# Optimization experiments

Measured on AMD Instinct MI355X. Metric: run time of the kernel, lower is better.

## Reference

```python
import jax, jax.numpy as jnp
import numpy as np


def _phi(z, conv_w, conv_b):
    # z: (H, W, S, 1) -> 3x3 SAME conv over state channels -> softmax over states
    x = jnp.transpose(z[..., 0], (2, 0, 1))[None]  # (1, S, H, W)
    y = jax.lax.conv_general_dilated(
        x, conv_w, window_strides=(1, 1), padding='SAME',
        dimension_numbers=('NCHW', 'OIHW', 'NCHW')) + conv_b[None, :, None, None]
    return jax.nn.softmax(jnp.transpose(y[0], (1, 2, 0)), axis=2)[..., None]  # (H, W, S, 1)


def _update(obs, P, u_k, w_k_O, conv_w, conv_b):
    H, W, O = obs.shape
    S = P.shape[0]
    # b = P^T @ obs per cell: b[h,w,s] = sum_o P[o,s] * obs[h,w,o]
    b = jnp.einsum('os,hwo->hws', P, obs)[..., None]  # (H, W, S, 1)
    # Analytic Jacobian db/dP: deriv_b[h,w,s,0,i,j] = obs[h,w,i] * delta(s==j)
    eye = jnp.eye(S, O, dtype=obs.dtype)
    deriv_b = (obs[:, :, None, :, None] * eye[None, None, :, None, :])[:, :, :, None, :, :]  # (H,W,S,1,S,O)

    Bu = b * u_k                                  # (H, W, S, 1)
    bu = jnp.sum(Bu, axis=2, keepdims=True)       # (H, W, 1, 1)
    Z = Bu / bu                                   # Bu / bu

    u_kp1 = _phi(Z, conv_w, conv_b)               # (H, W, S, 1)

    # Sensitivity recursion for obs params (quotient rule on Bu/bu)
    du = deriv_b * u_k[..., None, None] + b[..., None, None] * w_k_O  # (H,W,S,1,S,O)
    term1 = du * bu[..., None, None]
    term2 = jnp.expand_dims(jnp.sum(du, axis=2), 3) * Bu[..., None, None]
    w_pre = (term1 - term2) / bu[..., None, None] ** 2                # (H,W,S,1,S,O)

    # J @ w  ==  9 JVPs of Phi at Z with tangent columns of w (exact, avoids dense (HWS)^2 Jacobian)
    tangents = jnp.moveaxis(w_pre.reshape(H, W, S, 1, S * O), -1, 0)  # (S*O, H, W, S, 1)
    jvp1 = lambda t: jax.jvp(lambda z: _phi(z, conv_w, conv_b), (Z,), (t,))[1]
    w_kp1_O = jnp.moveaxis(jax.vmap(jvp1)(tangents), 0, -1).reshape(H, W, S, 1, S, O)
    return u_kp1, w_kp1_O


def setup_inputs() -> dict:
    key = jax.random.key(0)
    k1, k2, k3 = jax.random.split(key, 3)
    H = W = 512
    S = O = 3
    obs = jax.random.uniform(k1, (H, W, O), dtype=jnp.float32)
    obs_param_matrix = jnp.ones((S, O), jnp.float32) / O          # row-stochastic init
    u_k = jnp.ones((H, W, S, 1), jnp.float32) / S                 # uniform belief
    w_k_O = jnp.zeros((H, W, S, 1, S, O), jnp.float32)
    conv_w = jax.random.normal(k2, (S, S, 3, 3), jnp.float32) * 0.1
    conv_b = jax.random.normal(k3, (S,), jnp.float32) * 0.1
    return {'obs': obs, 'obs_param_matrix': obs_param_matrix, 'u_k': u_k,
            'w_k_O': w_k_O, 'conv_w': conv_w, 'conv_b': conv_b}


def reference(obs, obs_param_matrix, u_k, w_k_O, conv_w, conv_b):
    return _update(obs, obs_param_matrix, u_k, w_k_O, conv_w, conv_b)
```

## Files before the change

### kernel.cpp

```cpp
#include <hip/hip_runtime.h>

#define IMH 512
#define IMW 512
#define TW 32
#define TH 8
#define HW_ (TW + 2)
#define HH_ (TH + 2)
#define NHALO (HW_ * HH_)
#define ROW 31

__global__ __launch_bounds__(256, 2)
void hmm_fused(const float* __restrict__ obs,
               const float* __restrict__ P,
               const float* __restrict__ u_k,
               const float* __restrict__ w_k,
               const float* __restrict__ conv_w,
               const float* __restrict__ conv_b,
               float* __restrict__ out) {
    __shared__ float lds[NHALO * ROW];

    const int tid = threadIdx.x;
    const int w0 = blockIdx.x * TW;
    const int h0 = blockIdx.y * TH;

    float Pm[9];
#pragma unroll
    for (int i = 0; i < 9; ++i) Pm[i] = P[i];

    for (int p = tid; p < NHALO; p += 256) {
        const int hh = h0 + p / HW_ - 1;
        const int ww = w0 + p % HW_ - 1;
        float* row = &lds[p * ROW];
        if (hh < 0 || hh >= IMH || ww < 0 || ww >= IMW) {
#pragma unroll
            for (int c = 0; c < 30; ++c) row[c] = 0.0f;
            continue;
        }
        const int pix = hh * IMW + ww;
        const float ov[3] = {obs[pix * 3 + 0], obs[pix * 3 + 1], obs[pix * 3 + 2]};
        const float us[3] = {u_k[pix * 3 + 0], u_k[pix * 3 + 1], u_k[pix * 3 + 2]};

        float b[3], Bu[3], bu = 0.0f;
#pragma unroll
        for (int s = 0; s < 3; ++s) {
            b[s] = Pm[0 * 3 + s] * ov[0] + Pm[1 * 3 + s] * ov[1] + Pm[2 * 3 + s] * ov[2];
            Bu[s] = b[s] * us[s];
            bu += Bu[s];
        }
        const float inv_bu = 1.0f / bu;
        float Z[3];
#pragma unroll
        for (int s = 0; s < 3; ++s) { Z[s] = Bu[s] * inv_bu; row[s] = Z[s]; }

        const float* wkp = &w_k[(size_t)pix * 27];
#pragma unroll
        for (int i = 0; i < 3; ++i) {
#pragma unroll
            for (int j = 0; j < 3; ++j) {
                const int ij = i * 3 + j;
                float du[3], sdu = 0.0f;
#pragma unroll
                for (int s = 0; s < 3; ++s) {
                    float d = b[s] * wkp[s * 9 + ij];
                    if (s == j) d += ov[i] * us[s];
                    du[s] = d;
                    sdu += d;
                }
#pragma unroll
                for (int s = 0; s < 3; ++s)
                    row[(1 + ij) * 3 + s] = (du[s] - sdu * Z[s]) * inv_bu;
            }
        }
    }

    float cw[81];
#pragma unroll
    for (int i = 0; i < 81; ++i) cw[i] = conv_w[i];
    const float cb[3] = {conv_b[0], conv_b[1], conv_b[2]};

    __syncthreads();

    const int tx = tid % TW, ty = tid / TW;
    const int hp = (ty + 1) * HW_ + (tx + 1);
    const int pix = (h0 + ty) * IMW + (w0 + tx);

    float p0, p1, p2;
    {
        float y[3] = {cb[0], cb[1], cb[2]};
#pragma unroll
        for (int ky = 0; ky < 3; ++ky) {
#pragma unroll
            for (int kx = 0; kx < 3; ++kx) {
                const float* nb = &lds[(hp + (ky - 1) * HW_ + (kx - 1)) * ROW];
                const float v0 = nb[0], v1 = nb[1], v2 = nb[2];
#pragma unroll
                for (int s = 0; s < 3; ++s)
                    y[s] += cw[s * 27 + 0 * 9 + ky * 3 + kx] * v0 +
                            cw[s * 27 + 1 * 9 + ky * 3 + kx] * v1 +
                            cw[s * 27 + 2 * 9 + ky * 3 + kx] * v2;
            }
        }
        const float m = fmaxf(y[0], fmaxf(y[1], y[2]));
        const float e0 = __expf(y[0] - m), e1 = __expf(y[1] - m), e2 = __expf(y[2] - m);
        const float inv = 1.0f / (e0 + e1 + e2);
        p0 = e0 * inv; p1 = e1 * inv; p2 = e2 * inv;
        out[pix * 3 + 0] = p0; out[pix * 3 + 1] = p1; out[pix * 3 + 2] = p2;
    }

    float wout[27];
#pragma unroll
    for (int g = 1; g < 10; ++g) {
        float a[3] = {0.0f, 0.0f, 0.0f};
#pragma unroll
        for (int ky = 0; ky < 3; ++ky) {
#pragma unroll
            for (int kx = 0; kx < 3; ++kx) {
                const float* nb = &lds[(hp + (ky - 1) * HW_ + (kx - 1)) * ROW];
                const float v0 = nb[g * 3 + 0], v1 = nb[g * 3 + 1], v2 = nb[g * 3 + 2];
#pragma unroll
                for (int s = 0; s < 3; ++s)
                    a[s] += cw[s * 27 + 0 * 9 + ky * 3 + kx] * v0 +
                            cw[s * 27 + 1 * 9 + ky * 3 + kx] * v1 +
                            cw[s * 27 + 2 * 9 + ky * 3 + kx] * v2;
            }
        }
        const float dot = p0 * a[0] + p1 * a[1] + p2 * a[2];
        const int ij = g - 1;
        wout[0 * 9 + ij] = p0 * (a[0] - dot);
        wout[1 * 9 + ij] = p1 * (a[1] - dot);
        wout[2 * 9 + ij] = p2 * (a[2] - dot);
    }

    __syncthreads();

#pragma unroll
    for (int c = 0; c < 27; ++c) lds[tid * 27 + c] = wout[c];
    __syncthreads();

    float* outw = out + IMH * IMW * 3;
    for (int idx = tid; idx < TW * TH * 27; idx += 256) {
        const int r = idx / (TW * 27);
        const int rem = idx - r * (TW * 27);
        outw[(h0 + r) * (IMW * 27) + w0 * 27 + rem] = lds[idx];
    }
}

extern "C" void kernel_launch(void* const* d_in, const int* in_sizes, int n_in,
                              void* d_out, int out_size, void* d_ws, size_t ws_size,
                              hipStream_t stream) {
    const float* obs    = (const float*)d_in[0];
    const float* P      = (const float*)d_in[1];
    const float* u_k    = (const float*)d_in[2];
    const float* w_k    = (const float*)d_in[3];
    const float* conv_w = (const float*)d_in[4];
    const float* conv_b = (const float*)d_in[5];
    float* out = (float*)d_out;

    dim3 grid(IMW / TW, IMH / TH);
    hmm_fused<<<grid, 256, 0, stream>>>(obs, P, u_k, w_k, conv_w, conv_b, out);
}
```

Measured before the change: 109.5 us.

## Coalesce w_k staging via LDS, swizzle float4 layout, single-pass conv accumulation

```diff
diff --git a/kernel.cpp b/kernel.cpp
--- a/kernel.cpp
+++ b/kernel.cpp
@@ -3,13 +3,13 @@
 #define IMH 512
 #define IMW 512
 #define TW 32
-#define TH 8
+#define TH 16
 #define HW_ (TW + 2)
 #define HH_ (TH + 2)
 #define NHALO (HW_ * HH_)
-#define ROW 31
+#define NTHR 512
 
-__global__ __launch_bounds__(256, 2)
+__global__ __launch_bounds__(NTHR, 4)
 void hmm_fused(const float* __restrict__ obs,
                const float* __restrict__ P,
                const float* __restrict__ u_k,
@@ -17,7 +17,8 @@
                const float* __restrict__ conv_w,
                const float* __restrict__ conv_b,
                float* __restrict__ out) {
-    __shared__ float lds[NHALO * ROW];
+    __shared__ float4 lds4[NHALO * 8];
+    float* lds = (float*)lds4;
 
     const int tid = threadIdx.x;
     const int w0 = blockIdx.x * TW;
@@ -27,108 +28,141 @@
 #pragma unroll
     for (int i = 0; i < 9; ++i) Pm[i] = P[i];
 
-    for (int p = tid; p < NHALO; p += 256) {
-        const int hh = h0 + p / HW_ - 1;
-        const int ww = w0 + p % HW_ - 1;
-        float* row = &lds[p * ROW];
-        if (hh < 0 || hh >= IMH || ww < 0 || ww >= IMW) {
-#pragma unroll
-            for (int c = 0; c < 30; ++c) row[c] = 0.0f;
-            continue;
-        }
-        const int pix = hh * IMW + ww;
-        const float ov[3] = {obs[pix * 3 + 0], obs[pix * 3 + 1], obs[pix * 3 + 2]};
-        const float us[3] = {u_k[pix * 3 + 0], u_k[pix * 3 + 1], u_k[pix * 3 + 2]};
-
-        float b[3], Bu[3], bu = 0.0f;
-#pragma unroll
-        for (int s = 0; s < 3; ++s) {
-            b[s] = Pm[0 * 3 + s] * ov[0] + Pm[1 * 3 + s] * ov[1] + Pm[2 * 3 + s] * ov[2];
-            Bu[s] = b[s] * us[s];
-            bu += Bu[s];
-        }
-        const float inv_bu = 1.0f / bu;
-        float Z[3];
-#pragma unroll
-        for (int s = 0; s < 3; ++s) { Z[s] = Bu[s] * inv_bu; row[s] = Z[s]; }
-
-        const float* wkp = &w_k[(size_t)pix * 27];
-#pragma unroll
-        for (int i = 0; i < 3; ++i) {
-#pragma unroll
-            for (int j = 0; j < 3; ++j) {
-                const int ij = i * 3 + j;
-                float du[3], sdu = 0.0f;
-#pragma unroll
-                for (int s = 0; s < 3; ++s) {
-                    float d = b[s] * wkp[s * 9 + ij];
-                    if (s == j) d += ov[i] * us[s];
-                    du[s] = d;
-                    sdu += d;
-                }
-#pragma unroll
-                for (int s = 0; s < 3; ++s)
-                    row[(1 + ij) * 3 + s] = (du[s] - sdu * Z[s]) * inv_bu;
-            }
+    for (int r = 0; r < HH_; ++r) {
+        const int hh = h0 + r - 1;
+        if (hh < 0 || hh >= IMH) continue;
+        const long long gbase = ((long long)hh * IMW + (w0 - 1)) * 27;
+        for (int f = tid; f < HW_ * 27; f += NTHR) {
+            const int p = f / 27;
+            const int c = f - p * 27;
+            const int ww = w0 - 1 + p;
+            float v = 0.0f;
+            if (ww >= 0 && ww < IMW) v = w_k[gbase + f];
+            const int pr = r * HW_ + p;
+            lds[pr * 32 + (((c >> 2) + pr) & 7) * 4 + (c & 3)] = v;
         }
     }
 
     float cw[81];
 #pragma unroll
     for (int i = 0; i < 81; ++i) cw[i] = conv_w[i];
-    const float cb[3] = {conv_b[0], conv_b[1], conv_b[2]};
+    const float cb0 = conv_b[0], cb1 = conv_b[1], cb2 = conv_b[2];
 
     __syncthreads();
 
-    const int tx = tid % TW, ty = tid / TW;
-    const int hp = (ty + 1) * HW_ + (tx + 1);
-    const int pix = (h0 + ty) * IMW + (w0 + tx);
+    for (int p = tid; p < NHALO; p += NTHR) {
+        const int rr = p / HW_;
+        const int cc = p - rr * HW_;
+        const int hh = h0 + rr - 1;
+        const int ww = w0 + cc - 1;
+        float4 o[8];
+        if ((unsigned)hh < IMH && (unsigned)ww < IMW) {
+            float wv[28];
+#pragma unroll
+            for (int k = 0; k < 7; ++k) {
+                const float4 v = lds4[p * 8 + ((k + p) & 7)];
+                wv[4 * k + 0] = v.x; wv[4 * k + 1] = v.y;
+                wv[4 * k + 2] = v.z; wv[4 * k + 3] = v.w;
+            }
+            const int pix = hh * IMW + ww;
+            const float ov0 = obs[pix * 3 + 0], ov1 = obs[pix * 3 + 1], ov2 = obs[pix * 3 + 2];
+            const float us[3] = {u_k[pix * 3 + 0], u_k[pix * 3 + 1], u_k[pix * 3 + 2]};
 
-    float p0, p1, p2;
-    {
-        float y[3] = {cb[0], cb[1], cb[2]};
+            float b[3], Bu[3], bu = 0.0f;
 #pragma unroll
-        for (int ky = 0; ky < 3; ++ky) {
+            for (int s = 0; s < 3; ++s) {
+                b[s] = Pm[0 * 3 + s] * ov0 + Pm[1 * 3 + s] * ov1 + Pm[2 * 3 + s] * ov2;
+                Bu[s] = b[s] * us[s];
+                bu += Bu[s];
+            }
+            const float inv_bu = 1.0f / bu;
+            float Z[3], oc[32];
 #pragma unroll
-            for (int kx = 0; kx < 3; ++kx) {
-                const float* nb = &lds[(hp + (ky - 1) * HW_ + (kx - 1)) * ROW];
-                const float v0 = nb[0], v1 = nb[1], v2 = nb[2];
+            for (int s = 0; s < 3; ++s) { Z[s] = Bu[s] * inv_bu; oc[s] = Z[s]; }
+
+            const float ovv[3] = {ov0, ov1, ov2};
 #pragma unroll
-                for (int s = 0; s < 3; ++s)
-                    y[s] += cw[s * 27 + 0 * 9 + ky * 3 + kx] * v0 +
-                            cw[s * 27 + 1 * 9 + ky * 3 + kx] * v1 +
-                            cw[s * 27 + 2 * 9 + ky * 3 + kx] * v2;
+            for (int i = 0; i < 3; ++i) {
+#pragma unroll
+                for (int j = 0; j < 3; ++j) {
+                    const int ij = i * 3 + j;
+                    float du[3], sdu = 0.0f;
+#pragma unroll
+                    for (int s = 0; s < 3; ++s) {
+                        float d = b[s] * wv[s * 9 + ij];
+                        if (s == j) d += ovv[i] * us[s];
+                        du[s] = d;
+                        sdu += d;
+                    }
+#pragma unroll
+                    for (int s = 0; s < 3; ++s)
+                        oc[3 + ij * 3 + s] = (du[s] - sdu * Z[s]) * inv_bu;
+                }
+            }
+            oc[30] = 0.0f; oc[31] = 0.0f;
+#pragma unroll
+            for (int k = 0; k < 8; ++k)
+                o[k] = make_float4(oc[4 * k + 0], oc[4 * k + 1], oc[4 * k + 2], oc[4 * k + 3]);
+        } else {
+#pragma unroll
+            for (int k = 0; k < 8; ++k) o[k] = make_float4(0.f, 0.f, 0.f, 0.f);
+        }
+#pragma unroll
+        for (int k = 0; k < 8; ++k) lds4[p * 8 + ((k + p) & 7)] = o[k];
+    }
+
+    __syncthreads();
+
+    const int tx = tid & (TW - 1);
+    const int ty = tid >> 5;
+    const int hp = (ty + 1) * HW_ + tx + 1;
+
+    float acc[30];
+#pragma unroll
+    for (int i = 0; i < 30; ++i) acc[i] = 0.0f;
+
+#pragma unroll
+    for (int ky = 0; ky < 3; ++ky) {
+#pragma unroll
+        for (int kx = 0; kx < 3; ++kx) {
+            const int tap = ky * 3 + kx;
+            const int pn = hp + (ky - 1) * HW_ + (kx - 1);
+#pragma unroll
+            for (int k = 0; k < 8; ++k) {
+                const float4 v4 = lds4[pn * 8 + ((k + pn) & 7)];
+                const float cv[4] = {v4.x, v4.y, v4.z, v4.w};
+#pragma unroll
+                for (int j = 0; j < 4; ++j) {
+                    const int c = 4 * k + j;
+                    if (c < 30) {
+                        const int g = c / 3, si = c - (c / 3) * 3;
+                        acc[g * 3 + 0] += cw[0 * 27 + si * 9 + tap] * cv[j];
+                        acc[g * 3 + 1] += cw[1 * 27 + si * 9 + tap] * cv[j];
+                        acc[g * 3 + 2] += cw[2 * 27 + si * 9 + tap] * cv[j];
+                    }
+                }
             }
         }
-        const float m = fmaxf(y[0], fmaxf(y[1], y[2]));
-        const float e0 = __expf(y[0] - m), e1 = __expf(y[1] - m), e2 = __expf(y[2] - m);
-        const float inv = 1.0f / (e0 + e1 + e2);
-        p0 = e0 * inv; p1 = e1 * inv; p2 = e2 * inv;
-        out[pix * 3 + 0] = p0; out[pix * 3 + 1] = p1; out[pix * 3 + 2] = p2;
     }
+
+    const float y0 = acc[0] + cb0, y1 = acc[1] + cb1, y2 = acc[2] + cb2;
+    const float m = fmaxf(y0, fmaxf(y1, y2));
+    const float e0 = __expf(y0 - m), e1 = __expf(y1 - m), e2 = __expf(y2 - m);
+    const float inv = 1.0f / (e0 + e1 + e2);
+    const float p0 = e0 * inv, p1 = e1 * inv, p2 = e2 * inv;
+
+    const int pix = (h0 + ty) * IMW + (w0 + tx);
+    out[pix * 3 + 0] = p0; out[pix * 3 + 1] = p1; out[pix * 3 + 2] = p2;
 
     float wout[27];
 #pragma unroll
     for (int g = 1; g < 10; ++g) {
-        float a[3] = {0.0f, 0.0f, 0.0f};
-#pragma unroll
-        for (int ky = 0; ky < 3; ++ky) {
-#pragma unroll
-            for (int kx = 0; kx < 3; ++kx) {
-                const float* nb = &lds[(hp + (ky - 1) * HW_ + (kx - 1)) * ROW];
-                const float v0 = nb[g * 3 + 0], v1 = nb[g * 3 + 1], v2 = nb[g * 3 + 2];
-#pragma unroll
-                for (int s = 0; s < 3; ++s)
-                    a[s] += cw[s * 27 + 0 * 9 + ky * 3 + kx] * v0 +
-                            cw[s * 27 + 1 * 9 + ky * 3 + kx] * v1 +
-                            cw[s * 27 + 2 * 9 + ky * 3 + kx] * v2;
-            }
-        }
-        const float dot = p0 * a[0] + p1 * a[1] + p2 * a[2];
+        const float a0 = acc[g * 3 + 0], a1 = acc[g * 3 + 1], a2 = acc[g * 3 + 2];
+        const float dot = p0 * a0 + p1 * a1 + p2 * a2;
         const int ij = g - 1;
-        wout[0 * 9 + ij] = p0 * (a[0] - dot);
-        wout[1 * 9 + ij] = p1 * (a[1] - dot);
-        wout[2 * 9 + ij] = p2 * (a[2] - dot);
+        wout[0 * 9 + ij] = p0 * (a0 - dot);
+        wout[1 * 9 + ij] = p1 * (a1 - dot);
+        wout[2 * 9 + ij] = p2 * (a2 - dot);
     }
 
     __syncthreads();
@@ -138,10 +172,12 @@
     __syncthreads();
 
     float* outw = out + IMH * IMW * 3;
-    for (int idx = tid; idx < TW * TH * 27; idx += 256) {
-        const int r = idx / (TW * 27);
-        const int rem = idx - r * (TW * 27);
-        outw[(h0 + r) * (IMW * 27) + w0 * 27 + rem] = lds[idx];
+    for (int idx = tid; idx < TW * TH * 27 / 4; idx += NTHR) {
+        const int r = idx / 216;
+        const int q = idx - r * 216;
+        const float4 v = lds4[r * 216 + q];
+        float4* dst = (float4*)(outw + ((size_t)(h0 + r) * IMW + w0) * 27);
+        dst[q] = v;
     }
 }
 
@@ -157,5 +193,5 @@
     float* out = (float*)d_out;
 
     dim3 grid(IMW / TW, IMH / TH);
-    hmm_fused<<<grid, 256, 0, stream>>>(obs, P, u_k, w_k, conv_w, conv_b, out);
+    hmm_fused<<<grid, NTHR, 0, stream>>>(obs, P, u_k, w_k, conv_w, conv_b, out);
 }
```

After: 125.6 us. +14.7%, slower.

## Split fused kernel into pointwise pass and planar-workspace conv pass

Applied to the files above, without the earlier changes.

```diff
diff --git a/kernel.cpp b/kernel.cpp
--- a/kernel.cpp
+++ b/kernel.cpp
@@ -2,146 +2,126 @@
 
 #define IMH 512
 #define IMW 512
-#define TW 32
-#define TH 8
-#define HW_ (TW + 2)
-#define HH_ (TH + 2)
-#define NHALO (HW_ * HH_)
-#define ROW 31
+#define NPIX (IMH * IMW)
+#define RS 516
+#define PR 514
+#define PLANE (PR * RS)
+#define NCH 30
+#define NBORD 2052
 
-__global__ __launch_bounds__(256, 2)
-void hmm_fused(const float* __restrict__ obs,
-               const float* __restrict__ P,
-               const float* __restrict__ u_k,
-               const float* __restrict__ w_k,
-               const float* __restrict__ conv_w,
-               const float* __restrict__ conv_b,
-               float* __restrict__ out) {
-    __shared__ float lds[NHALO * ROW];
+__global__ __launch_bounds__(256)
+void k1_pointwise(const float* __restrict__ obs,
+                  const float* __restrict__ P,
+                  const float* __restrict__ u_k,
+                  const float* __restrict__ w_k,
+                  float* __restrict__ ws) {
+    const int gtid = blockIdx.x * 256 + threadIdx.x;
 
-    const int tid = threadIdx.x;
-    const int w0 = blockIdx.x * TW;
-    const int h0 = blockIdx.y * TH;
+    for (int i = gtid; i < NCH * NBORD; i += NPIX) {
+        const int pl = i / NBORD, r = i - pl * NBORD;
+        int rr, cc;
+        if (r < 514)       { rr = 0;            cc = r; }
+        else if (r < 1028) { rr = 513;          cc = r - 514; }
+        else if (r < 1540) { rr = r - 1028 + 1; cc = 0; }
+        else               { rr = r - 1540 + 1; cc = 513; }
+        ws[(size_t)pl * PLANE + rr * RS + cc] = 0.0f;
+    }
 
-    float Pm[9];
+    const int h = gtid >> 9, w = gtid & 511;
+    const float ov[3] = {obs[gtid*3+0], obs[gtid*3+1], obs[gtid*3+2]};
+    const float us[3] = {u_k[gtid*3+0], u_k[gtid*3+1], u_k[gtid*3+2]};
+
+    float b[3], Bu[3], bu = 0.0f;
 #pragma unroll
-    for (int i = 0; i < 9; ++i) Pm[i] = P[i];
+    for (int s = 0; s < 3; ++s) {
+        b[s] = P[s] * ov[0] + P[3+s] * ov[1] + P[6+s] * ov[2];
+        Bu[s] = b[s] * us[s];
+        bu += Bu[s];
+    }
+    const float inv_bu = 1.0f / bu;
+    float Z[3];
+#pragma unroll
+    for (int s = 0; s < 3; ++s) Z[s] = Bu[s] * inv_bu;
 
-    for (int p = tid; p < NHALO; p += 256) {
-        const int hh = h0 + p / HW_ - 1;
-        const int ww = w0 + p % HW_ - 1;
-        float* row = &lds[p * ROW];
-        if (hh < 0 || hh >= IMH || ww < 0 || ww >= IMW) {
+    const int base = (h + 1) * RS + (w + 1);
+    ws[0*PLANE + base] = Z[0];
+    ws[1*PLANE + base] = Z[1];
+    ws[2*PLANE + base] = Z[2];
+
+    const float* wk = w_k + (size_t)gtid * 27;
+    float wv[27];
 #pragma unroll
-            for (int c = 0; c < 30; ++c) row[c] = 0.0f;
-            continue;
-        }
-        const int pix = hh * IMW + ww;
-        const float ov[3] = {obs[pix * 3 + 0], obs[pix * 3 + 1], obs[pix * 3 + 2]};
-        const float us[3] = {u_k[pix * 3 + 0], u_k[pix * 3 + 1], u_k[pix * 3 + 2]};
+    for (int c = 0; c < 27; ++c) wv[c] = wk[c];
 
-        float b[3], Bu[3], bu = 0.0f;
+#pragma unroll
+    for (int ij = 0; ij < 9; ++ij) {
+        const int i = ij / 3, j = ij % 3;
+        float du[3], sdu = 0.0f;
 #pragma unroll
         for (int s = 0; s < 3; ++s) {
-            b[s] = Pm[0 * 3 + s] * ov[0] + Pm[1 * 3 + s] * ov[1] + Pm[2 * 3 + s] * ov[2];
-            Bu[s] = b[s] * us[s];
-            bu += Bu[s];
+            float d = b[s] * wv[s*9 + ij];
+            if (s == j) d += ov[i] * us[s];
+            du[s] = d;
+            sdu += d;
         }
-        const float inv_bu = 1.0f / bu;
-        float Z[3];
 #pragma unroll
-        for (int s = 0; s < 3; ++s) { Z[s] = Bu[s] * inv_bu; row[s] = Z[s]; }
+        for (int s = 0; s < 3; ++s)
+            ws[(size_t)(3 + ij*3 + s) * PLANE + base] = (du[s] - sdu * Z[s]) * inv_bu;
+    }
+}
 
-        const float* wkp = &w_k[(size_t)pix * 27];
-#pragma unroll
-        for (int i = 0; i < 3; ++i) {
-#pragma unroll
-            for (int j = 0; j < 3; ++j) {
-                const int ij = i * 3 + j;
-                float du[3], sdu = 0.0f;
-#pragma unroll
-                for (int s = 0; s < 3; ++s) {
-                    float d = b[s] * wkp[s * 9 + ij];
-                    if (s == j) d += ov[i] * us[s];
-                    du[s] = d;
-                    sdu += d;
-                }
-#pragma unroll
-                for (int s = 0; s < 3; ++s)
-                    row[(1 + ij) * 3 + s] = (du[s] - sdu * Z[s]) * inv_bu;
-            }
-        }
-    }
+__global__ __launch_bounds__(256)
+void k2_conv(const float* __restrict__ ws,
+             const float* __restrict__ conv_w,
+             const float* __restrict__ conv_b,
+             float* __restrict__ out) {
+    const int gtid = blockIdx.x * 256 + threadIdx.x;
+    const int h = gtid >> 9, w = gtid & 511;
 
     float cw[81];
 #pragma unroll
     for (int i = 0; i < 81; ++i) cw[i] = conv_w[i];
-    const float cb[3] = {conv_b[0], conv_b[1], conv_b[2]};
+    const float cb0 = conv_b[0], cb1 = conv_b[1], cb2 = conv_b[2];
 
-    __syncthreads();
+    const int base = h * RS + w;
 
-    const int tx = tid % TW, ty = tid / TW;
-    const int hp = (ty + 1) * HW_ + (tx + 1);
-    const int pix = (h0 + ty) * IMW + (w0 + tx);
+    float acc[30];
+#pragma unroll
+    for (int i = 0; i < 30; ++i) acc[i] = 0.0f;
 
-    float p0, p1, p2;
-    {
-        float y[3] = {cb[0], cb[1], cb[2]};
+#pragma unroll
+    for (int c = 0; c < NCH; ++c) {
+        const int g = c / 3, si = c - g * 3;
+        const float* pl = ws + (size_t)c * PLANE + base;
 #pragma unroll
         for (int ky = 0; ky < 3; ++ky) {
-#pragma unroll
-            for (int kx = 0; kx < 3; ++kx) {
-                const float* nb = &lds[(hp + (ky - 1) * HW_ + (kx - 1)) * ROW];
-                const float v0 = nb[0], v1 = nb[1], v2 = nb[2];
-#pragma unroll
-                for (int s = 0; s < 3; ++s)
-                    y[s] += cw[s * 27 + 0 * 9 + ky * 3 + kx] * v0 +
-                            cw[s * 27 + 1 * 9 + ky * 3 + kx] * v1 +
-                            cw[s * 27 + 2 * 9 + ky * 3 + kx] * v2;
-            }
+            const float v0 = pl[ky*RS + 0];
+            const float v1 = pl[ky*RS + 1];
+            const float v2 = pl[ky*RS + 2];
+            const int t = si * 9 + ky * 3;
+            acc[g*3+0] += cw[0*27 + t] * v0 + cw[0*27 + t + 1] * v1 + cw[0*27 + t + 2] * v2;
+            acc[g*3+1] += cw[1*27 + t] * v0 + cw[1*27 + t + 1] * v1 + cw[1*27 + t + 2] * v2;
+            acc[g*3+2] += cw[2*27 + t] * v0 + cw[2*27 + t + 1] * v1 + cw[2*27 + t + 2] * v2;
         }
-        const float m = fmaxf(y[0], fmaxf(y[1], y[2]));
-        const float e0 = __expf(y[0] - m), e1 = __expf(y[1] - m), e2 = __expf(y[2] - m);
-        const float inv = 1.0f / (e0 + e1 + e2);
-        p0 = e0 * inv; p1 = e1 * inv; p2 = e2 * inv;
-        out[pix * 3 + 0] = p0; out[pix * 3 + 1] = p1; out[pix * 3 + 2] = p2;
     }
 
-    float wout[27];
+    const float y0 = acc[0] + cb0, y1 = acc[1] + cb1, y2 = acc[2] + cb2;
+    const float m = fmaxf(y0, fmaxf(y1, y2));
+    const float e0 = __expf(y0 - m), e1 = __expf(y1 - m), e2 = __expf(y2 - m);
+    const float inv = 1.0f / (e0 + e1 + e2);
+    const float p0 = e0 * inv, p1 = e1 * inv, p2 = e2 * inv;
+
+    out[gtid*3 + 0] = p0; out[gtid*3 + 1] = p1; out[gtid*3 + 2] = p2;
+
+    float* outw = out + (size_t)NPIX * 3 + (size_t)gtid * 27;
 #pragma unroll
     for (int g = 1; g < 10; ++g) {
-        float a[3] = {0.0f, 0.0f, 0.0f};
-#pragma unroll
-        for (int ky = 0; ky < 3; ++ky) {
-#pragma unroll
-            for (int kx = 0; kx < 3; ++kx) {
-                const float* nb = &lds[(hp + (ky - 1) * HW_ + (kx - 1)) * ROW];
-                const float v0 = nb[g * 3 + 0], v1 = nb[g * 3 + 1], v2 = nb[g * 3 + 2];
-#pragma unroll
-                for (int s = 0; s < 3; ++s)
-                    a[s] += cw[s * 27 + 0 * 9 + ky * 3 + kx] * v0 +
-                            cw[s * 27 + 1 * 9 + ky * 3 + kx] * v1 +
-                            cw[s * 27 + 2 * 9 + ky * 3 + kx] * v2;
-            }
-        }
-        const float dot = p0 * a[0] + p1 * a[1] + p2 * a[2];
+        const float a0 = acc[g*3+0], a1 = acc[g*3+1], a2 = acc[g*3+2];
+        const float dot = p0*a0 + p1*a1 + p2*a2;
         const int ij = g - 1;
-        wout[0 * 9 + ij] = p0 * (a[0] - dot);
-        wout[1 * 9 + ij] = p1 * (a[1] - dot);
-        wout[2 * 9 + ij] = p2 * (a[2] - dot);
-    }
-
-    __syncthreads();
-
-#pragma unroll
-    for (int c = 0; c < 27; ++c) lds[tid * 27 + c] = wout[c];
-    __syncthreads();
-
-    float* outw = out + IMH * IMW * 3;
-    for (int idx = tid; idx < TW * TH * 27; idx += 256) {
-        const int r = idx / (TW * 27);
-        const int rem = idx - r * (TW * 27);
-        outw[(h0 + r) * (IMW * 27) + w0 * 27 + rem] = lds[idx];
+        outw[0*9 + ij] = p0 * (a0 - dot);
+        outw[1*9 + ij] = p1 * (a1 - dot);
+        outw[2*9 + ij] = p2 * (a2 - dot);
     }
 }
 
@@ -155,7 +135,9 @@
     const float* conv_w = (const float*)d_in[4];
     const float* conv_b = (const float*)d_in[5];
     float* out = (float*)d_out;
+    float* ws  = (float*)d_ws;
 
-    dim3 grid(IMW / TW, IMH / TH);
-    hmm_fused<<<grid, 256, 0, stream>>>(obs, P, u_k, w_k, conv_w, conv_b, out);
+    const int nblk = NPIX / 256;
+    k1_pointwise<<<nblk, 256, 0, stream>>>(obs, P, u_k, w_k, ws);
+    k2_conv<<<nblk, 256, 0, stream>>>(ws, conv_w, conv_b, out);
 }
```

Result: slower. 149.3 us (+36.3%).
